# Optimization experiments

Hardware: AMD Instinct MI355X
Metric: run time of the kernel (lower is better)

The kernel has to match this reference:

```python
import jax, jax.numpy as jnp
import numpy as np

S, B, E, H = 2048, 4, 1024, 16
D = E // H


def setup_inputs() -> dict:
    key = jax.random.key(0)
    ks = jax.random.split(key, 12)
    scale = 1.0 / np.sqrt(E)
    inp = {
        "query": jax.random.normal(ks[0], (S, B, E), jnp.float32),
        "key": jax.random.normal(ks[1], (S, B, E), jnp.float32),
        "value": jax.random.normal(ks[2], (S, B, E), jnp.float32),
        # causal mask: True = masked out (matches masked_fill semantics)
        "attn_mask": jnp.triu(jnp.ones((S, S), jnp.bool_), k=1),
        "Wq": jax.random.normal(ks[3], (E, E), jnp.float32) * scale,
        "bq": jax.random.normal(ks[4], (E,), jnp.float32) * scale,
        "Wk": jax.random.normal(ks[5], (E, E), jnp.float32) * scale,
        "bk": jax.random.normal(ks[6], (E,), jnp.float32) * scale,
        "Wv": jax.random.normal(ks[7], (E, E), jnp.float32) * scale,
        "bv": jax.random.normal(ks[8], (E,), jnp.float32) * scale,
        "Wo": jax.random.normal(ks[9], (E, E), jnp.float32) * scale,
        "bo": jax.random.normal(ks[10], (E,), jnp.float32) * scale,
    }
    return inp


def reference(query, key, value, attn_mask, Wq, bq, Wk, bk, Wv, bv, Wo, bo):
    # inputs are [S, B, E]; torch Linear: y = x @ W.T + b
    def proj_heads(x, W, b):
        y = jnp.einsum("sbe,fe->sbf", x, W) + b          # [S,B,E]
        return y.transpose(1, 0, 2).reshape(B, S, H, D).transpose(0, 2, 1, 3)  # [B,H,S,D]

    Q = proj_heads(query, Wq, bq)
    K = proj_heads(key, Wk, bk)
    V = proj_heads(value, Wv, bv)

    scores = jnp.einsum("bhsd,bhtd->bhst", Q, K) / jnp.sqrt(jnp.float32(D))
    scores = jnp.where(attn_mask[None, None, :, :], -jnp.inf, scores)
    probs = jax.nn.softmax(scores, axis=-1)              # dropout p=0 -> identity

    ctx = jnp.einsum("bhst,bhtd->bhsd", probs, V)        # [B,H,S,D]
    ctx = ctx.transpose(0, 2, 1, 3).reshape(B, S, E).transpose(1, 0, 2)  # [S,B,E]

    out = jnp.einsum("sbe,fe->sbf", ctx, Wo) + bo        # [S,B,E]
    attn_map = probs.mean(axis=1)                        # [B,S,S]
    return out, attn_map
```

## Files before the change

### kernel.cpp

```cpp
#include <hip/hip_runtime.h>
#include <stdint.h>

#define S_LEN 2048
#define B_SZ  4
#define E_SZ  1024
#define H_CNT 16
#define D_HD  64

typedef __attribute__((ext_vector_type(4))) float          f32x4;
typedef __attribute__((ext_vector_type(2))) float          f32x2;
typedef __attribute__((ext_vector_type(8))) __bf16         bf16x8;
typedef __attribute__((ext_vector_type(4))) unsigned short u16x4;
typedef __attribute__((ext_vector_type(4))) int            i32x4;
typedef __attribute__((ext_vector_type(2))) int            i32x2;
typedef unsigned short us;

#define QSCALE 0.1803368801111204f

__device__ __forceinline__ us bfu(float f) {
    __bf16 h = (__bf16)f;
    return __builtin_bit_cast(us, h);
}
__device__ __forceinline__ unsigned pk2(float a, float b) {
    return (unsigned)bfu(a) | ((unsigned)bfu(b) << 16);
}
#define EXP2(x) __builtin_amdgcn_exp2f(x)
#define MFMA(a, b, c) __builtin_amdgcn_mfma_f32_16x16x32_bf16((a), (b), (c), 0, 0, 0)

__device__ __forceinline__ void gll16(const void* g, void* l) {
    __builtin_amdgcn_global_load_lds(
        (const __attribute__((address_space(1))) void*)g,
        (__attribute__((address_space(3))) void*)l, 16, 0, 0);
}

__global__ __launch_bounds__(256)
void convert_many(const float* __restrict__ s0, const float* __restrict__ s1,
                  const float* __restrict__ s2, const float* __restrict__ s3,
                  us* __restrict__ d0, us* __restrict__ d1,
                  us* __restrict__ d2, us* __restrict__ d3,
                  float sc0)
{
    const int which = blockIdx.y;
    const float* s = which == 0 ? s0 : which == 1 ? s1 : which == 2 ? s2 : s3;
    us* d = which == 0 ? d0 : which == 1 ? d1 : which == 2 ? d2 : d3;
    const float sc = which == 0 ? sc0 : 1.0f;
    const int i = blockIdx.x * 256 + threadIdx.x;
    f32x4 v = ((const f32x4*)s)[i];
    u16x4 o;
    o.x = bfu(v.x * sc); o.y = bfu(v.y * sc);
    o.z = bfu(v.z * sc); o.w = bfu(v.w * sc);
    ((u16x4*)d)[i] = o;
}

template<bool AF32, bool OUT_QKV>
__global__ __launch_bounds__(256)
void gemm_bt(const void* __restrict__ Ap,
             const us* __restrict__ Bw,
             const float* __restrict__ bias, float bscale,
             void* __restrict__ Outp)
{
    __shared__ us Al[2][128 * 64];
    __shared__ us Bl[2][128 * 64];

    const int t     = threadIdx.x;
    const int lane  = t & 63;
    const int wave  = t >> 6;
    const int lrow  = lane & 15;
    const int lk    = lane >> 4;
    const int xq    = blockIdx.x & 7;
    const int kq    = blockIdx.x >> 3;
    const int bm    = ((kq & 56) | xq) << 7;
    const int bn    = (kq & 7) << 7;
    const int wr    = (wave >> 1) << 6;
    const int wc    = (wave & 1) << 6;
    const int srow8 = lane >> 3;
    const int scol  = (lane & 7) << 3;

    f32x4 acc[4][4];
    #pragma unroll
    for (int i = 0; i < 4; ++i)
        #pragma unroll
        for (int j = 0; j < 4; ++j) acc[i][j] = (f32x4)0.0f;

    #define GSTAGE(k0_, dst_)                                                        \
        _Pragma("unroll")                                                            \
        for (int j_ = 0; j_ < 4; ++j_) {                                             \
            const int chunk_ = wave * 4 + j_;                                        \
            const int r_ = chunk_ * 8 + srow8;                                       \
            gll16((const us*)Ap + (size_t)(bm + r_) * E_SZ + (k0_) + scol,           \
                  &Al[dst_][chunk_ * 512]);                                          \
            gll16(Bw + (size_t)(bn + r_) * E_SZ + (k0_) + scol,                      \
                  &Bl[dst_][chunk_ * 512]);                                          \
        }

    #define GCOMP(src_)                                                              \
        _Pragma("unroll")                                                            \
        for (int kk = 0; kk < 2; ++kk) {                                             \
            bf16x8 af[4], bfr[4];                                                    \
            _Pragma("unroll")                                                        \
            for (int i = 0; i < 4; ++i)                                              \
                af[i] = *(const bf16x8*)(&Al[src_][(wr + i*16 + lrow) * 64 + kk*32 + lk*8]); \
            _Pragma("unroll")                                                        \
            for (int j = 0; j < 4; ++j)                                              \
                bfr[j] = *(const bf16x8*)(&Bl[src_][(wc + j*16 + lrow) * 64 + kk*32 + lk*8]); \
            _Pragma("unroll")                                                        \
            for (int i = 0; i < 4; ++i)                                              \
                _Pragma("unroll")                                                    \
                for (int j = 0; j < 4; ++j)                                          \
                    acc[i][j] = MFMA(af[i], bfr[j], acc[i][j]);                      \
        }

    if (AF32) {
        for (int k0 = 0; k0 < E_SZ; k0 += 64) {
            __syncthreads();
            #pragma unroll
            for (int j = 0; j < 4; ++j) {
                const int chunk = wave * 4 + j;
                const int r = chunk * 8 + srow8;
                const float* ga = (const float*)Ap + (size_t)(bm + r) * E_SZ + k0 + scol;
                f32x4 u0 = *(const f32x4*)ga;
                f32x4 u1 = *(const f32x4*)(ga + 4);
                i32x4 wv;
                wv.x = (int)pk2(u0.x, u0.y); wv.y = (int)pk2(u0.z, u0.w);
                wv.z = (int)pk2(u1.x, u1.y); wv.w = (int)pk2(u1.z, u1.w);
                *(i32x4*)(&Al[0][chunk * 512 + lane * 8]) = wv;
                gll16(Bw + (size_t)(bn + r) * E_SZ + k0 + scol, &Bl[0][chunk * 512]);
            }
            __syncthreads();
            GCOMP(0);
        }
    } else {
        GSTAGE(0, 0);
        __syncthreads();
        int buf = 0;
        #pragma unroll 2
        for (int kt = 0; kt < 15; ++kt) {
            GSTAGE((kt + 1) * 64, buf ^ 1);
            GCOMP(buf);
            __syncthreads();
            buf ^= 1;
        }
        GCOMP(buf);
    }
    #undef GSTAGE
    #undef GCOMP

    const int crow = lk << 2;
    #pragma unroll
    for (int i = 0; i < 4; ++i) {
        #pragma unroll
        for (int j = 0; j < 4; ++j) {
            const int n = bn + wc + j*16 + lrow;
            const float bv = bias[n] * bscale;
            #pragma unroll
            for (int r = 0; r < 4; ++r) {
                const int m = bm + wr + i*16 + crow + r;
                const float val = acc[i][j][r] + bv;
                if (OUT_QKV) {
                    const int s = m >> 2, b = m & 3;
                    const int h = n >> 6, d = n & 63;
                    ((us*)Outp)[((size_t)(b*H_CNT + h)*S_LEN + s)*D_HD + d] = bfu(val);
                } else {
                    ((float*)Outp)[(size_t)m * E_SZ + n] = val;
                }
            }
        }
    }
}

__global__ __launch_bounds__(512, 6)
void flash_fwd(const us* __restrict__ Qb,
               const us* __restrict__ Kb,
               const us* __restrict__ Vb,
               us* __restrict__ ctx,
               float* __restrict__ lout)
{
    __shared__ us Kl[2][64 * 64];
    __shared__ us Vt[2][64 * 72];
    __shared__ us Pl[8][16 * 72];

    const int t    = threadIdx.x;
    const int lane = t & 63, wave = t >> 6;
    const int lrow = lane & 15, lk = lane >> 4;
    const int bh   = blockIdx.x & 63;
    const int qt   = 15 - (blockIdx.x >> 6);
    const int b    = bh >> 4, h = bh & 15;

    const size_t base = (size_t)bh * S_LEN * D_HD;
    const us* Q = Qb + base;
    const us* K = Kb + base;
    const us* V = Vb + base;

    const int qbase = qt * 128 + wave * 16;
    const int myq   = qbase + lrow;
    us* pl = &Pl[wave][0];

    bf16x8 qf[2];
    #pragma unroll
    for (int ks = 0; ks < 2; ++ks)
        qf[ks] = *(const bf16x8*)(Q + (size_t)myq * D_HD + ks*32 + lk*8);

    f32x4 ctxa[4];
    #pragma unroll
    for (int nf = 0; nf < 4; ++nf) ctxa[nf] = (f32x4)0.0f;
    float lst = 0.0f;

    const int tU  = t & 255;
    const int vp2 = (tU & 31) << 1;
    const int vd8 = (tU >> 5) << 3;

    i32x4 v0, v1;

    #define STAGE_K(kv_, kl_)                                                        \
        if (t < 256) {                                                               \
            _Pragma("unroll")                                                        \
            for (int i_ = 0; i_ < 2; ++i_) {                                         \
                const int row_  = i_*32 + (t >> 3);                                  \
                const int slot_ = (t & 7) ^ (row_ & 7);                              \
                gll16(K + (size_t)((kv_) + row_)*D_HD + slot_*8,                     \
                      (kl_) + i_*2048 + ((t >> 6) << 9));                            \
            }                                                                        \
        }
    #define LOAD_V(kv_)                                                             \
        if (t >= 256) {                                                              \
            const us* vp_ = V + (size_t)((kv_) + vp2)*D_HD + vd8;                    \
            v0 = *(const i32x4*)vp_;                                                 \
            v1 = *(const i32x4*)(vp_ + D_HD);                                        \
        }
    #define WRITE_V(vt_)                                                             \
        if (t >= 256) {                                                              \
            union { i32x4 v; us s[8]; } ua_, ub_; ua_.v = v0; ub_.v = v1;            \
            _Pragma("unroll")                                                        \
            for (int j_ = 0; j_ < 8; ++j_) {                                         \
                unsigned w_ = (unsigned)ua_.s[j_] | ((unsigned)ub_.s[j_] << 16);     \
                *(unsigned*)((vt_) + (vd8 + j_)*72 + vp2) = w_;                      \
            }                                                                        \
        }

    STAGE_K(0, Kl[0]);
    LOAD_V(0);
    WRITE_V(Vt[0]);
    __syncthreads();

    const int kvend = qt*128 + 128;
    int cur = 0;
    for (int kv = 0; kv < kvend; kv += 64) {
        const bool more = (kv + 64) < kvend;
        if (more) {
            STAGE_K(kv + 64, Kl[cur ^ 1]);
            LOAD_V(kv + 64);
        }

        if (kv <= qbase) {
            const us* kl = Kl[cur];
            const us* vt = Vt[cur];
            f32x4 sa[4];
            #pragma unroll
            for (int nf = 0; nf < 4; ++nf) sa[nf] = (f32x4)0.0f;
            #pragma unroll
            for (int ks = 0; ks < 2; ++ks)
                #pragma unroll
                for (int nf = 0; nf < 4; ++nf) {
                    const int key = nf*16 + lrow;
                    bf16x8 kf = *(const bf16x8*)((const char*)kl + (key << 7) +
                                    (((((ks << 2) | lk)) ^ (lrow & 7)) << 4));
                    sa[nf] = MFMA(kf, qf[ks], sa[nf]);
                }
            if (kv + 63 > qbase) {
                #pragma unroll
                for (int nf = 0; nf < 4; ++nf)
                    #pragma unroll
                    for (int r = 0; r < 4; ++r)
                        if (kv + nf*16 + (lk << 2) + r > myq) sa[nf][r] = -__builtin_inff();
            }
            float sum = 0.0f;
            #pragma unroll
            for (int nf = 0; nf < 4; ++nf)
                #pragma unroll
                for (int r = 0; r < 4; ++r) {
                    const float p = EXP2(sa[nf][r]);
                    sa[nf][r] = p;
                    sum += p;
                }
            sum += __shfl_xor(sum, 16);
            sum += __shfl_xor(sum, 32);
            lst += sum;
            #pragma unroll
            for (int nf = 0; nf < 4; ++nf) {
                i32x2 dw;
                dw.x = (int)pk2(sa[nf][0], sa[nf][1]);
                dw.y = (int)pk2(sa[nf][2], sa[nf][3]);
                *(i32x2*)(pl + lrow*72 + nf*16 + (lk << 2)) = dw;
            }
            #pragma unroll
            for (int ks = 0; ks < 2; ++ks) {
                bf16x8 pa = *(const bf16x8*)(pl + lrow*72 + ks*32 + lk*8);
                #pragma unroll
                for (int nf = 0; nf < 4; ++nf) {
                    bf16x8 vf = *(const bf16x8*)(vt + (nf*16 + lrow)*72 + ks*32 + lk*8);
                    ctxa[nf] = MFMA(pa, vf, ctxa[nf]);
                }
            }
        }

        if (more) { WRITE_V(Vt[cur ^ 1]); }
        __syncthreads();
        cur ^= 1;
    }

    const float inv = 1.0f / lst;
    float invr[4];
    #pragma unroll
    for (int r = 0; r < 4; ++r) invr[r] = __shfl(inv, (lk << 2) + r);
    #pragma unroll
    for (int nf = 0; nf < 4; ++nf)
        #pragma unroll
        for (int r = 0; r < 4; ++r) {
            const int srow = qbase + (lk << 2) + r;
            const int d    = nf*16 + lrow;
            ctx[((size_t)srow * B_SZ + b) * E_SZ + h*D_HD + d] = bfu(ctxa[nf][r] * invr[r]);
        }
    if (lane < 16)
        lout[(size_t)bh * S_LEN + myq] = inv * 0.0625f;
    #undef STAGE_K
    #undef LOAD_V
    #undef WRITE_V
}

__global__ __launch_bounds__(512, 4)
void attn_map_k(const us* __restrict__ Qb,
                const us* __restrict__ Kb,
                const float* __restrict__ lrows,
                float* __restrict__ map)
{
    const int t  = threadIdx.x;
    const int xq = blockIdx.x & 7;
    const int rq = blockIdx.x >> 3;
    const int p  = ((rq >> 4) << 3) | xq;
    const int jt = rq & 15;
    const int it = p & 15;
    const int b  = p >> 4;
    float* mt = map + ((size_t)b * S_LEN + it*128) * S_LEN + jt*128;

    if (jt > it) {
        f32x4 z = (f32x4)0.0f;
        #pragma unroll
        for (int i = 0; i < 8; ++i) {
            const int c = i*512 + t;
            *(f32x4*)(mt + (size_t)(c >> 5) * S_LEN + (c & 31) * 4) = z;
        }
        return;
    }

    __shared__ us Ql[128 * 64];
    __shared__ us Kl[128 * 64];
    __shared__ float Ll[16 * 128];

    const int lane = t & 63, wave = t >> 6;
    const int lrow = lane & 15, lk = lane >> 4;
    const int wr = (wave >> 1) << 5;
    const int wc = (wave & 1) << 6;

    #pragma unroll
    for (int i = 0; i < 4; ++i) {
        const int idx = i*512 + t;
        const int h = idx >> 7, row = idx & 127;
        Ll[idx] = lrows[(size_t)(b*H_CNT + h)*S_LEN + it*128 + row];
    }

    f32x4 pacc[2][4];
    #pragma unroll
    for (int i = 0; i < 2; ++i)
        #pragma unroll
        for (int j = 0; j < 4; ++j) pacc[i][j] = (f32x4)0.0f;

    const int qrow  = it*128;
    const int krow  = jt*128;
    const int srow  = t >> 3;
    const int sslot = t & 7;

    for (int h = 0; h < H_CNT; ++h) {
        const size_t base = (size_t)(b*H_CNT + h) * S_LEN * D_HD;
        const us* Qh = Qb + base + (size_t)qrow * D_HD;
        const us* Kh = Kb + base + (size_t)krow * D_HD;
        __syncthreads();
        #pragma unroll
        for (int i = 0; i < 2; ++i) {
            const int row  = i*64 + srow;
            const int slot = sslot ^ (row & 7);
            gll16(Qh + (size_t)row * D_HD + slot*8, &Ql[i*4096 + ((t >> 6) << 9)]);
            gll16(Kh + (size_t)row * D_HD + slot*8, &Kl[i*4096 + ((t >> 6) << 9)]);
        }
        __syncthreads();

        bf16x8 kf[4][2];
        #pragma unroll
        for (int nf = 0; nf < 4; ++nf)
            #pragma unroll
            for (int ks = 0; ks < 2; ++ks) {
                const int row = wc + nf*16 + lrow;
                kf[nf][ks] = *(const bf16x8*)(&Kl[row*64 + (((ks<<2)|lk) ^ (row&7))*8]);
            }

        #pragma unroll
        for (int mf = 0; mf < 2; ++mf) {
            const int arow = wr + mf*16 + lrow;
            bf16x8 af0 = *(const bf16x8*)(&Ql[arow*64 + ((lk)     ^ (arow&7))*8]);
            bf16x8 af1 = *(const bf16x8*)(&Ql[arow*64 + ((4 | lk) ^ (arow&7))*8]);
            float lv[4];
            #pragma unroll
            for (int r = 0; r < 4; ++r)
                lv[r] = Ll[h*128 + wr + mf*16 + (lk << 2) + r];
            #pragma unroll
            for (int nf = 0; nf < 4; ++nf) {
                f32x4 sa = (f32x4)0.0f;
                sa = MFMA(af0, kf[nf][0], sa);
                sa = MFMA(af1, kf[nf][1], sa);
                #pragma unroll
                for (int r = 0; r < 4; ++r)
                    pacc[mf][nf][r] += EXP2(sa[r]) * lv[r];
            }
        }
    }

    #pragma unroll
    for (int mf = 0; mf < 2; ++mf)
        #pragma unroll
        for (int nf = 0; nf < 4; ++nf)
            #pragma unroll
            for (int r = 0; r < 4; ++r) {
                const int row = wr + mf*16 + (lk << 2) + r;
                const int col = wc + nf*16 + lrow;
                float v = pacc[mf][nf][r];
                if (it == jt && col > row) v = 0.0f;
                mt[(size_t)row * S_LEN + col] = v;
            }
}

extern "C" void kernel_launch(void* const* d_in, const int* in_sizes, int n_in,
                              void* d_out, int out_size, void* d_ws, size_t ws_size,
                              hipStream_t stream)
{
    const float* q_in = (const float*)d_in[0];
    const float* k_in = (const float*)d_in[1];
    const float* v_in = (const float*)d_in[2];
    const float* Wq = (const float*)d_in[4];
    const float* bq = (const float*)d_in[5];
    const float* Wk = (const float*)d_in[6];
    const float* bk = (const float*)d_in[7];
    const float* Wv = (const float*)d_in[8];
    const float* bv = (const float*)d_in[9];
    const float* Wo = (const float*)d_in[10];
    const float* bo = (const float*)d_in[11];

    const size_t EE   = (size_t)E_SZ * E_SZ;
    const size_t BHSD = (size_t)B_SZ * H_CNT * S_LEN * D_HD;
    const size_t SBE  = (size_t)S_LEN * B_SZ * E_SZ;

    us* Wqb = (us*)d_ws;
    us* Wkb = Wqb + EE;
    us* Wvb = Wkb + EE;
    us* Wob = Wvb + EE;
    us* base = Wob + EE;

    const size_t need_big = (4*EE + 6*BHSD) * sizeof(us);
    const bool big = ws_size >= need_big;

    us *Aq, *Ak, *Av, *Qb, *Kb, *Vb, *ctx;
    float* ml;
    if (big) {
        Aq = base;       Ak = Aq + BHSD;  Av = Ak + BHSD;
        Qb = Av + BHSD;  Kb = Qb + BHSD;  Vb = Kb + BHSD;
        ctx = Aq;
        ml  = (float*)Ak;
    } else {
        Aq = Ak = Av = nullptr;
        Qb = base;       Kb = Qb + BHSD;  Vb = Kb + BHSD;
        ctx = Vb + BHSD;
        ml  = (float*)(ctx + SBE);
    }
    float* lrows = ml;

    float* out = (float*)d_out;
    float* map = out + SBE;

    convert_many<<<dim3(1024, 4), 256, 0, stream>>>(Wq, Wk, Wv, Wo, Wqb, Wkb, Wvb, Wob, QSCALE);

    if (big) {
        convert_many<<<dim3(8192, 3), 256, 0, stream>>>(q_in, k_in, v_in, nullptr,
                                                        Aq, Ak, Av, nullptr, 1.0f);
        gemm_bt<false, true><<<512, 256, 0, stream>>>(Aq, Wqb, bq, QSCALE, Qb);
        gemm_bt<false, true><<<512, 256, 0, stream>>>(Ak, Wkb, bk, 1.0f,   Kb);
        gemm_bt<false, true><<<512, 256, 0, stream>>>(Av, Wvb, bv, 1.0f,   Vb);
    } else {
        gemm_bt<true, true><<<512, 256, 0, stream>>>(q_in, Wqb, bq, QSCALE, Qb);
        gemm_bt<true, true><<<512, 256, 0, stream>>>(k_in, Wkb, bk, 1.0f,   Kb);
        gemm_bt<true, true><<<512, 256, 0, stream>>>(v_in, Wvb, bv, 1.0f,   Vb);
    }

    flash_fwd<<<1024, 512, 0, stream>>>(Qb, Kb, Vb, ctx, lrows);

    gemm_bt<false, false><<<512, 256, 0, stream>>>(ctx, Wob, bo, 1.0f, d_out);

    attn_map_k<<<B_SZ*16*16, 512, 0, stream>>>(Qb, Kb, lrows, map);
}
```

Baseline: 243.6 us.

## Merge convert and QKV GEMM launches; read Q fragments directly in attn-map kernel

Weight and activation bf16 conversions now run as one kernel launch, and the three QKV projection GEMMs run as a single 1536-block launch that selects operands by block index. This cuts launch overhead and tail effects between kernels. In the attention-map kernel, the Q tile is no longer staged into LDS each head; each wave loads its Q fragments straight from global memory. That frees LDS and removes a copy, but the global reads are uncoalesced. The output GEMM's epilogue switch is now a runtime bool instead of a template parameter.

New measurement: 269.9 us. 1.11x slower.

```diff
diff --git a/kernel.cpp b/kernel.cpp
--- a/kernel.cpp
+++ b/kernel.cpp
@@ -34,17 +34,29 @@
 }
 
 __global__ __launch_bounds__(256)
-void convert_many(const float* __restrict__ s0, const float* __restrict__ s1,
-                  const float* __restrict__ s2, const float* __restrict__ s3,
-                  us* __restrict__ d0, us* __restrict__ d1,
-                  us* __restrict__ d2, us* __restrict__ d3,
-                  float sc0)
+void convert_all(const float* __restrict__ qi, const float* __restrict__ ki,
+                 const float* __restrict__ vi,
+                 const float* __restrict__ Wq, const float* __restrict__ Wk,
+                 const float* __restrict__ Wv, const float* __restrict__ Wo,
+                 us* __restrict__ dq, us* __restrict__ dk, us* __restrict__ dv,
+                 us* __restrict__ dWq, us* __restrict__ dWk,
+                 us* __restrict__ dWv, us* __restrict__ dWo)
 {
-    const int which = blockIdx.y;
-    const float* s = which == 0 ? s0 : which == 1 ? s1 : which == 2 ? s2 : s3;
-    us* d = which == 0 ? d0 : which == 1 ? d1 : which == 2 ? d2 : d3;
-    const float sc = which == 0 ? sc0 : 1.0f;
-    const int i = blockIdx.x * 256 + threadIdx.x;
+    const int bid = blockIdx.x;
+    const float* s; us* d; float sc = 1.0f; size_t i;
+    if (bid < 4096) {
+        const int w = bid >> 10;
+        s = w == 0 ? Wq : w == 1 ? Wk : w == 2 ? Wv : Wo;
+        d = w == 0 ? dWq : w == 1 ? dWk : w == 2 ? dWv : dWo;
+        if (w == 0) sc = QSCALE;
+        i = (size_t)(bid & 1023) * 256 + threadIdx.x;
+    } else {
+        const int r = bid - 4096;
+        const int w = r >> 13;
+        s = w == 0 ? qi : w == 1 ? ki : vi;
+        d = w == 0 ? dq : w == 1 ? dk : dv;
+        i = (size_t)(r & 8191) * 256 + threadIdx.x;
+    }
     f32x4 v = ((const f32x4*)s)[i];
     u16x4 o;
     o.x = bfu(v.x * sc); o.y = bfu(v.y * sc);
@@ -52,29 +64,83 @@
     ((u16x4*)d)[i] = o;
 }
 
-template<bool AF32, bool OUT_QKV>
+#define GEMM_DECLS                                                                   \
+    const int t     = threadIdx.x;                                                   \
+    const int lane  = t & 63;                                                        \
+    const int wave  = t >> 6;                                                        \
+    const int lrow  = lane & 15;                                                     \
+    const int lk    = lane >> 4;                                                     \
+    const int xq    = bid & 7;                                                       \
+    const int kq    = bid >> 3;                                                      \
+    const int bm    = ((kq & 56) | xq) << 7;                                         \
+    const int bn    = (kq & 7) << 7;                                                 \
+    const int wr    = (wave >> 1) << 6;                                              \
+    const int wc    = (wave & 1) << 6;                                               \
+    const int srow8 = lane >> 3;                                                     \
+    const int scol  = (lane & 7) << 3;
+
+#define GSTAGE(k0_, dst_)                                                            \
+    _Pragma("unroll")                                                                \
+    for (int j_ = 0; j_ < 4; ++j_) {                                                 \
+        const int chunk_ = wave * 4 + j_;                                            \
+        const int r_ = chunk_ * 8 + srow8;                                           \
+        gll16((const us*)Ap + (size_t)(bm + r_) * E_SZ + (k0_) + scol,               \
+              &Al[dst_][chunk_ * 512]);                                              \
+        gll16(Bw + (size_t)(bn + r_) * E_SZ + (k0_) + scol,                          \
+              &Bl[dst_][chunk_ * 512]);                                              \
+    }
+
+#define GCOMP(src_)                                                                  \
+    _Pragma("unroll")                                                                \
+    for (int kk = 0; kk < 2; ++kk) {                                                 \
+        bf16x8 af[4], bfr[4];                                                        \
+        _Pragma("unroll")                                                            \
+        for (int i = 0; i < 4; ++i)                                                  \
+            af[i] = *(const bf16x8*)(&Al[src_][(wr + i*16 + lrow) * 64 + kk*32 + lk*8]); \
+        _Pragma("unroll")                                                            \
+        for (int j = 0; j < 4; ++j)                                                  \
+            bfr[j] = *(const bf16x8*)(&Bl[src_][(wc + j*16 + lrow) * 64 + kk*32 + lk*8]); \
+        _Pragma("unroll")                                                            \
+        for (int i = 0; i < 4; ++i)                                                  \
+            _Pragma("unroll")                                                        \
+            for (int j = 0; j < 4; ++j)                                              \
+                acc[i][j] = MFMA(af[i], bfr[j], acc[i][j]);                          \
+    }
+
+#define GEMM_MAIN_BF16                                                               \
+    GSTAGE(0, 0);                                                                    \
+    __syncthreads();                                                                 \
+    int buf = 0;                                                                     \
+    _Pragma("unroll 2")                                                              \
+    for (int kt = 0; kt < 15; ++kt) {                                                \
+        GSTAGE((kt + 1) * 64, buf ^ 1);                                              \
+        GCOMP(buf);                                                                  \
+        __syncthreads();                                                             \
+        buf ^= 1;                                                                    \
+    }                                                                                \
+    GCOMP(buf);
+
 __global__ __launch_bounds__(256)
-void gemm_bt(const void* __restrict__ Ap,
-             const us* __restrict__ Bw,
-             const float* __restrict__ bias, float bscale,
-             void* __restrict__ Outp)
+void gemm_qkv(const us* __restrict__ Aq, const us* __restrict__ Ak,
+              const us* __restrict__ Av,
+              const us* __restrict__ Wqb, const us* __restrict__ Wkb,
+              const us* __restrict__ Wvb,
+              const float* __restrict__ bq, const float* __restrict__ bk,
+              const float* __restrict__ bv,
+              us* __restrict__ Qb, us* __restrict__ Kb, us* __restrict__ Vb)
 {
     __shared__ us Al[2][128 * 64];
     __shared__ us Bl[2][128 * 64];
 
-    const int t     = threadIdx.x;
-    const int lane  = t & 63;
-    const int wave  = t >> 6;
-    const int lrow  = lane & 15;
-    const int lk    = lane >> 4;
-    const int xq    = blockIdx.x & 7;
-    const int kq    = blockIdx.x >> 3;
-    const int bm    = ((kq & 56) | xq) << 7;
-    const int bn    = (kq & 7) << 7;
-    const int wr    = (wave >> 1) << 6;
-    const int wc    = (wave & 1) << 6;
-    const int srow8 = lane >> 3;
-    const int scol  = (lane & 7) << 3;
+    const int which = blockIdx.x >> 9;
+    const int bid   = blockIdx.x & 511;
+    const us* Ap    = which == 0 ? Aq : which == 1 ? Ak : Av;
+    const us* Bw    = which == 0 ? Wqb : which == 1 ? Wkb : Wvb;
+    const float* bias = which == 0 ? bq : which == 1 ? bk : bv;
+    us* Out         = which == 0 ? Qb : which == 1 ? Kb : Vb;
+    const float bscale = which == 0 ? QSCALE : 1.0f;
+
+    GEMM_DECLS
 
     f32x4 acc[4][4];
     #pragma unroll
@@ -82,33 +148,45 @@
         #pragma unroll
         for (int j = 0; j < 4; ++j) acc[i][j] = (f32x4)0.0f;
 
-    #define GSTAGE(k0_, dst_)                                                        \
-        _Pragma("unroll")                                                            \
-        for (int j_ = 0; j_ < 4; ++j_) {                                             \
-            const int chunk_ = wave * 4 + j_;                                        \
-            const int r_ = chunk_ * 8 + srow8;                                       \
-            gll16((const us*)Ap + (size_t)(bm + r_) * E_SZ + (k0_) + scol,           \
-                  &Al[dst_][chunk_ * 512]);                                          \
-            gll16(Bw + (size_t)(bn + r_) * E_SZ + (k0_) + scol,                      \
-                  &Bl[dst_][chunk_ * 512]);                                          \
-        }
-
-    #define GCOMP(src_)                                                              \
-        _Pragma("unroll")                                                            \
-        for (int kk = 0; kk < 2; ++kk) {                                             \
-            bf16x8 af[4], bfr[4];                                                    \
-            _Pragma("unroll")                                                        \
-            for (int i = 0; i < 4; ++i)                                              \
-                af[i] = *(const bf16x8*)(&Al[src_][(wr + i*16 + lrow) * 64 + kk*32 + lk*8]); \
-            _Pragma("unroll")                                                        \
-            for (int j = 0; j < 4; ++j)                                              \
-                bfr[j] = *(const bf16x8*)(&Bl[src_][(wc + j*16 + lrow) * 64 + kk*32 + lk*8]); \
-            _Pragma("unroll")                                                        \
-            for (int i = 0; i < 4; ++i)                                              \
-                _Pragma("unroll")                                                    \
-                for (int j = 0; j < 4; ++j)                                          \
-                    acc[i][j] = MFMA(af[i], bfr[j], acc[i][j]);                      \
-        }
+    GEMM_MAIN_BF16
+
+    const int crow = lk << 2;
+    #pragma unroll
+    for (int i = 0; i < 4; ++i) {
+        #pragma unroll
+        for (int j = 0; j < 4; ++j) {
+            const int n = bn + wc + j*16 + lrow;
+            const float bvv = bias[n] * bscale;
+            #pragma unroll
+            for (int r = 0; r < 4; ++r) {
+                const int m = bm + wr + i*16 + crow + r;
+                const float val = acc[i][j][r] + bvv;
+                const int s = m >> 2, b = m & 3;
+                const int h = n >> 6, d = n & 63;
+                Out[((size_t)(b*H_CNT + h)*S_LEN + s)*D_HD + d] = bfu(val);
+            }
+        }
+    }
+}
+
+template<bool AF32>
+__global__ __launch_bounds__(256)
+void gemm_out(const void* __restrict__ Ap,
+              const us* __restrict__ Bw,
+              const float* __restrict__ bias, float bscale,
+              void* __restrict__ Outp, bool out_qkv)
+{
+    __shared__ us Al[2][128 * 64];
+    __shared__ us Bl[2][128 * 64];
+
+    const int bid = blockIdx.x;
+    GEMM_DECLS
+
+    f32x4 acc[4][4];
+    #pragma unroll
+    for (int i = 0; i < 4; ++i)
+        #pragma unroll
+        for (int j = 0; j < 4; ++j) acc[i][j] = (f32x4)0.0f;
 
     if (AF32) {
         for (int k0 = 0; k0 < E_SZ; k0 += 64) {
@@ -130,20 +208,8 @@
             GCOMP(0);
         }
     } else {
-        GSTAGE(0, 0);
-        __syncthreads();
-        int buf = 0;
-        #pragma unroll 2
-        for (int kt = 0; kt < 15; ++kt) {
-            GSTAGE((kt + 1) * 64, buf ^ 1);
-            GCOMP(buf);
-            __syncthreads();
-            buf ^= 1;
-        }
-        GCOMP(buf);
-    }
-    #undef GSTAGE
-    #undef GCOMP
+        GEMM_MAIN_BF16
+    }
 
     const int crow = lk << 2;
     #pragma unroll
@@ -151,12 +217,12 @@
         #pragma unroll
         for (int j = 0; j < 4; ++j) {
             const int n = bn + wc + j*16 + lrow;
-            const float bv = bias[n] * bscale;
+            const float bvv = bias[n] * bscale;
             #pragma unroll
             for (int r = 0; r < 4; ++r) {
                 const int m = bm + wr + i*16 + crow + r;
-                const float val = acc[i][j][r] + bv;
-                if (OUT_QKV) {
+                const float val = acc[i][j][r] + bvv;
+                if (out_qkv) {
                     const int s = m >> 2, b = m & 3;
                     const int h = n >> 6, d = n & 63;
                     ((us*)Outp)[((size_t)(b*H_CNT + h)*S_LEN + s)*D_HD + d] = bfu(val);
@@ -352,7 +418,6 @@
         return;
     }
 
-    __shared__ us Ql[128 * 64];
     __shared__ us Kl[128 * 64];
     __shared__ float Ll[16 * 128];
 
@@ -381,14 +446,13 @@
 
     for (int h = 0; h < H_CNT; ++h) {
         const size_t base = (size_t)(b*H_CNT + h) * S_LEN * D_HD;
-        const us* Qh = Qb + base + (size_t)qrow * D_HD;
         const us* Kh = Kb + base + (size_t)krow * D_HD;
+        const us* Qg = Qb + base + (size_t)(qrow + wr) * D_HD;
         __syncthreads();
         #pragma unroll
         for (int i = 0; i < 2; ++i) {
             const int row  = i*64 + srow;
             const int slot = sslot ^ (row & 7);
-            gll16(Qh + (size_t)row * D_HD + slot*8, &Ql[i*4096 + ((t >> 6) << 9)]);
             gll16(Kh + (size_t)row * D_HD + slot*8, &Kl[i*4096 + ((t >> 6) << 9)]);
         }
         __syncthreads();
@@ -404,9 +468,9 @@
 
         #pragma unroll
         for (int mf = 0; mf < 2; ++mf) {
-            const int arow = wr + mf*16 + lrow;
-            bf16x8 af0 = *(const bf16x8*)(&Ql[arow*64 + ((lk)     ^ (arow&7))*8]);
-            bf16x8 af1 = *(const bf16x8*)(&Ql[arow*64 + ((4 | lk) ^ (arow&7))*8]);
+            const us* qp = Qg + (size_t)(mf*16 + lrow) * D_HD;
+            bf16x8 af0 = *(const bf16x8*)(qp + lk*8);
+            bf16x8 af1 = *(const bf16x8*)(qp + 32 + lk*8);
             float lv[4];
             #pragma unroll
             for (int r = 0; r < 4; ++r)
@@ -484,23 +548,24 @@
     float* out = (float*)d_out;
     float* map = out + SBE;
 
-    convert_many<<<dim3(1024, 4), 256, 0, stream>>>(Wq, Wk, Wv, Wo, Wqb, Wkb, Wvb, Wob, QSCALE);
-
     if (big) {
-        convert_many<<<dim3(8192, 3), 256, 0, stream>>>(q_in, k_in, v_in, nullptr,
-                                                        Aq, Ak, Av, nullptr, 1.0f);
-        gemm_bt<false, true><<<512, 256, 0, stream>>>(Aq, Wqb, bq, QSCALE, Qb);
-        gemm_bt<false, true><<<512, 256, 0, stream>>>(Ak, Wkb, bk, 1.0f,   Kb);
-        gemm_bt<false, true><<<512, 256, 0, stream>>>(Av, Wvb, bv, 1.0f,   Vb);
+        convert_all<<<4096 + 3*8192, 256, 0, stream>>>(
+            q_in, k_in, v_in, Wq, Wk, Wv, Wo,
+            Aq, Ak, Av, Wqb, Wkb, Wvb, Wob);
+        gemm_qkv<<<1536, 256, 0, stream>>>(Aq, Ak, Av, Wqb, Wkb, Wvb,
+                                           bq, bk, bv, Qb, Kb, Vb);
     } else {
-        gemm_bt<true, true><<<512, 256, 0, stream>>>(q_in, Wqb, bq, QSCALE, Qb);
-        gemm_bt<true, true><<<512, 256, 0, stream>>>(k_in, Wkb, bk, 1.0f,   Kb);
-        gemm_bt<true, true><<<512, 256, 0, stream>>>(v_in, Wvb, bv, 1.0f,   Vb);
+        convert_all<<<4096, 256, 0, stream>>>(
+            q_in, k_in, v_in, Wq, Wk, Wv, Wo,
+            nullptr, nullptr, nullptr, Wqb, Wkb, Wvb, Wob);
+        gemm_out<true><<<512, 256, 0, stream>>>(q_in, Wqb, bq, QSCALE, Qb, true);
+        gemm_out<true><<<512, 256, 0, stream>>>(k_in, Wkb, bk, 1.0f,   Kb, true);
+        gemm_out<true><<<512, 256, 0, stream>>>(v_in, Wvb, bv, 1.0f,   Vb, true);
     }
 
     flash_fwd<<<1024, 512, 0, stream>>>(Qb, Kb, Vb, ctx, lrows);
 
-    gemm_bt<false, false><<<512, 256, 0, stream>>>(ctx, Wob, bo, 1.0f, d_out);
+    gemm_out<false><<<512, 256, 0, stream>>>(ctx, Wob, bo, 1.0f, d_out, false);
 
     attn_map_k<<<B_SZ*16*16, 512, 0, stream>>>(Qb, Kb, lrows, map);
 }
```
